# Kernel optimization log

Hardware: AMD Instinct MI355X
Metric: run time of the kernel (lower is better)

## Reference

```python
import jax, jax.numpy as jnp
import numpy as np

N = 50000      # points
K = 16         # neighbors per point
DIM = 256      # channels
H = 8          # heads
HD = DIM // H  # head dim


def setup_inputs() -> dict:
    key = jax.random.key(0)
    ks = jax.random.split(key, 8)
    feats = jax.random.normal(ks[0], (N, DIM), jnp.float32)
    xyz = jax.random.normal(ks[1], (N, 3), jnp.float32)
    # sorted segment ids: each point attends to exactly K neighbors
    index_0 = jnp.repeat(jnp.arange(N, dtype=jnp.int32), K)            # [M]
    index_1 = jax.random.randint(ks[2], (N * K,), 0, N, dtype=jnp.int32)  # [M]
    index_0_offsets = jnp.arange(N + 1, dtype=jnp.int32) * K
    s = 1.0 / np.sqrt(DIM)
    qkv_w = jax.random.normal(ks[3], (3 * DIM, DIM), jnp.float32) * s
    qkv_b = jax.random.normal(ks[4], (3 * DIM,), jnp.float32) * 0.01
    proj_w = jax.random.normal(ks[5], (DIM, DIM), jnp.float32) * s
    proj_b = jax.random.normal(ks[6], (DIM,), jnp.float32) * 0.01
    return {
        'feats': feats, 'xyz': xyz,
        'index_0': index_0, 'index_1': index_1,
        'index_0_offsets': index_0_offsets, 'n_max': K,
        'qkv_w': qkv_w, 'qkv_b': qkv_b, 'proj_w': proj_w, 'proj_b': proj_b,
    }


def reference(feats, xyz, index_0, index_1, index_0_offsets, n_max,
              qkv_w, qkv_b, proj_w, proj_b):
    n, c = feats.shape
    scale = (c // H) ** (-0.5)
    qkv = (feats @ qkv_w.T + qkv_b).reshape(n, 3, H, HD)  # [N,3,H,HD]
    q = qkv[:, 0] * scale
    k = qkv[:, 1]
    v = qkv[:, 2]
    # attention_step1: per-pair gathered dot product -> [M, H]
    attn = jnp.einsum('mhd,mhd->mh', q[index_0], k[index_1])
    # scatter_softmax over segments of index_0 (numerically stable)
    seg_max = jax.ops.segment_max(attn, index_0, num_segments=n)  # [N,H]
    e = jnp.exp(attn - seg_max[index_0])
    denom = jax.ops.segment_sum(e, index_0, num_segments=n)       # [N,H]
    attn = e / denom[index_0]                                     # [M,H]
    # attention_step2: scatter weighted sum of gathered values -> [N,H,HD]
    x = jax.ops.segment_sum(attn[:, :, None] * v[index_1], index_0,
                            num_segments=n)
    x = x.reshape(n, c)
    return x @ proj_w.T + proj_b
```

## Files before the change

### kernel.cpp

```cpp
#include <hip/hip_runtime.h>
#include <hip/hip_bf16.h>
#include <stdint.h>

typedef __bf16 bf16x8_t __attribute__((ext_vector_type(8)));
typedef float f32x4_t __attribute__((ext_vector_type(4)));

__device__ __forceinline__ float b2f(unsigned short u) {
    union { uint32_t i; float f; } x; x.i = ((uint32_t)u) << 16; return x.f;
}
__device__ __forceinline__ unsigned short f2b(float f) {
    union { float f; uint32_t i; } x; x.f = f;
    uint32_t r = (x.i + 0x7fffu + ((x.i >> 16) & 1u)) >> 16;
    return (unsigned short)r;
}

__global__ void cvt_f32_bf16(const float* __restrict__ in, unsigned short* __restrict__ out, int n) {
    int i = (blockIdx.x * blockDim.x + threadIdx.x) * 4;
    if (i >= n) return;
    const float4 v = *reinterpret_cast<const float4*>(in + i);
    ushort4 o;
    o.x = f2b(v.x); o.y = f2b(v.y); o.z = f2b(v.z); o.w = f2b(v.w);
    *reinterpret_cast<ushort4*>(out + i) = o;
}

template <bool OUT_BF16>
__launch_bounds__(256, 2)
__global__ void gemm_bf16(const unsigned short* __restrict__ A,
                          const unsigned short* __restrict__ W,
                          const float* __restrict__ bias,
                          void* __restrict__ Cout,
                          int M, int Nn, int Kk) {
    const int nCol = Nn >> 7;
    const int p = blockIdx.x;
    const int xcd = p & 7;
    const int q = p >> 3;
    const int c = q % nCol;
    const int rr = q / nCol;
    const int r = rr * 8 + xcd;
    const int blockRow = r * 128;
    if (blockRow >= M) return;
    const int blockCol = c * 128;

    __shared__ unsigned short As[128 * 64];
    __shared__ unsigned short Bs[128 * 64];
    const int t = threadIdx.x;
    const int w = t >> 6;
    const int l = t & 63;
    const int wm = w >> 1, wn = w & 1;

    f32x4_t acc[4][4];
#pragma unroll
    for (int i = 0; i < 4; ++i)
#pragma unroll
        for (int j = 0; j < 4; ++j) acc[i][j] = (f32x4_t)0.f;

    const int srow = t >> 3;
    const int scol = (t & 7) * 8;

    for (int k0 = 0; k0 < Kk; k0 += 64) {
#pragma unroll
        for (int cc = 0; cc < 4; ++cc) {
            int arow = blockRow + cc * 32 + srow;
            arow = arow < M ? arow : M - 1;
            const unsigned short* ga = A + (size_t)arow * Kk + k0 + scol;
            const int brow = blockCol + cc * 32 + srow;
            const unsigned short* gb = W + (size_t)brow * Kk + k0 + scol;
            unsigned short* la = &As[cc * 2048 + w * 512];
            unsigned short* lb = &Bs[cc * 2048 + w * 512];
            __builtin_amdgcn_global_load_lds((const __attribute__((address_space(1))) void*)ga,
                                             (__attribute__((address_space(3))) void*)la, 16, 0, 0);
            __builtin_amdgcn_global_load_lds((const __attribute__((address_space(1))) void*)gb,
                                             (__attribute__((address_space(3))) void*)lb, 16, 0, 0);
        }
        __syncthreads();
#pragma unroll
        for (int kc = 0; kc < 2; ++kc) {
            bf16x8_t af[4], bfr[4];
            const int kof = kc * 32 + (l >> 4) * 8;
#pragma unroll
            for (int i = 0; i < 4; ++i) {
                af[i]  = *reinterpret_cast<const bf16x8_t*>(&As[(wm * 64 + i * 16 + (l & 15)) * 64 + kof]);
                bfr[i] = *reinterpret_cast<const bf16x8_t*>(&Bs[(wn * 64 + i * 16 + (l & 15)) * 64 + kof]);
            }
#pragma unroll
            for (int i = 0; i < 4; ++i)
#pragma unroll
                for (int j = 0; j < 4; ++j)
                    acc[i][j] = __builtin_amdgcn_mfma_f32_16x16x32_bf16(af[i], bfr[j], acc[i][j], 0, 0, 0);
        }
        __syncthreads();
    }

    const int lr = (l >> 4) * 4;
    const int lc = l & 15;
#pragma unroll
    for (int i = 0; i < 4; ++i) {
#pragma unroll
        for (int j = 0; j < 4; ++j) {
            const int col = blockCol + wn * 64 + j * 16 + lc;
            const float bz = bias[col];
#pragma unroll
            for (int rg = 0; rg < 4; ++rg) {
                const int row = blockRow + wm * 64 + i * 16 + lr + rg;
                if (row < M) {
                    const float val = acc[i][j][rg] + bz;
                    if (OUT_BF16)
                        ((unsigned short*)Cout)[(size_t)row * Nn + col] = f2b(val);
                    else
                        ((float*)Cout)[(size_t)row * Nn + col] = val;
                }
            }
        }
    }
}

__global__ void attn_bf16(const unsigned short* __restrict__ qkv,
                          const int* __restrict__ index_1,
                          unsigned short* __restrict__ x) {
    const int w = threadIdx.x >> 6;
    const int i = blockIdx.x * 4 + w;
    const int l = threadIdx.x & 63;
    const int h = l >> 3;
    const int d0 = (l & 7) * 4;
    const float scale = 0.17677669529663687f;

    int nbr[16];
#pragma unroll
    for (int m = 0; m < 16; ++m) nbr[m] = index_1[i * 16 + m];

    ushort4 kreg[16], vreg[16];
#pragma unroll
    for (int m = 0; m < 16; ++m) {
        const unsigned short* base = qkv + (size_t)nbr[m] * 768 + 256 + h * 32 + d0;
        kreg[m] = *reinterpret_cast<const ushort4*>(base);
        vreg[m] = *reinterpret_cast<const ushort4*>(base + 256);
    }

    const ushort4 qu = *reinterpret_cast<const ushort4*>(&qkv[(size_t)i * 768 + h * 32 + d0]);
    const float qx = b2f(qu.x) * scale, qy = b2f(qu.y) * scale,
                qz = b2f(qu.z) * scale, qw = b2f(qu.w) * scale;

    float s[16];
#pragma unroll
    for (int m = 0; m < 16; ++m) {
        float p = qx * b2f(kreg[m].x) + qy * b2f(kreg[m].y)
                + qz * b2f(kreg[m].z) + qw * b2f(kreg[m].w);
        p += __shfl_xor(p, 1, 8);
        p += __shfl_xor(p, 2, 8);
        p += __shfl_xor(p, 4, 8);
        s[m] = p;
    }
    float mx = -1e30f;
#pragma unroll
    for (int m = 0; m < 16; ++m) mx = fmaxf(mx, s[m]);
    float sum = 0.f;
#pragma unroll
    for (int m = 0; m < 16; ++m) { s[m] = __expf(s[m] - mx); sum += s[m]; }
    const float inv = 1.f / sum;

    float ax = 0.f, ay = 0.f, az = 0.f, aw = 0.f;
#pragma unroll
    for (int m = 0; m < 16; ++m) {
        const float wt = s[m] * inv;
        ax += wt * b2f(vreg[m].x); ay += wt * b2f(vreg[m].y);
        az += wt * b2f(vreg[m].z); aw += wt * b2f(vreg[m].w);
    }
    ushort4 o;
    o.x = f2b(ax); o.y = f2b(ay); o.z = f2b(az); o.w = f2b(aw);
    *reinterpret_cast<ushort4*>(&x[(size_t)i * 256 + h * 32 + d0]) = o;
}

extern "C" void kernel_launch(void* const* d_in, const int* in_sizes, int n_in,
                              void* d_out, int out_size, void* d_ws, size_t ws_size,
                              hipStream_t stream) {
    const float* feats   = (const float*)d_in[0];
    const int*   index_1 = (const int*)d_in[3];
    const float* qkv_w   = (const float*)d_in[6];
    const float* qkv_b   = (const float*)d_in[7];
    const float* proj_w  = (const float*)d_in[8];
    const float* proj_b  = (const float*)d_in[9];
    float* out = (float*)d_out;

    const int N = 50000, DIM = 256, QKVD = 768;

    unsigned short* featsb = (unsigned short*)d_ws;
    unsigned short* qkvwb  = featsb + (size_t)N * DIM;
    unsigned short* projwb = qkvwb + (size_t)QKVD * DIM;
    unsigned short* qkvb   = projwb + (size_t)DIM * DIM;
    unsigned short* xb     = qkvb + (size_t)N * QKVD;

    cvt_f32_bf16<<<(N * DIM / 4 + 255) / 256, 256, 0, stream>>>(feats, featsb, N * DIM);
    cvt_f32_bf16<<<(QKVD * DIM / 4 + 255) / 256, 256, 0, stream>>>(qkv_w, qkvwb, QKVD * DIM);
    cvt_f32_bf16<<<(DIM * DIM / 4 + 255) / 256, 256, 0, stream>>>(proj_w, projwb, DIM * DIM);

    const int nRow = (N + 127) / 128;
    const int nRowPad = ((nRow + 7) / 8) * 8;

    gemm_bf16<true><<<nRowPad * (QKVD / 128), 256, 0, stream>>>(featsb, qkvwb, qkv_b, qkvb, N, QKVD, DIM);
    attn_bf16<<<N / 4, 256, 0, stream>>>(qkvb, index_1, xb);
    gemm_bf16<false><<<nRowPad * (DIM / 128), 256, 0, stream>>>(xb, projwb, proj_b, out, N, DIM, DIM);
}
```

Measured before the change: 309.7 us.

## Split QKV into separate planes and attention into logits and output kernels

The QKV GEMM now writes Q, K and V to three separate contiguous [N,256] bf16 arrays, so each gathered row comes from a smaller array. The attention kernel is split in two: one computes softmax weights from gathered K and stores them as packed bf16, the other gathers V and accumulates the weighted sum. The softmax scale is folded into the Q weights and bias inside a merged weight-prep kernel, and the weights are kept in bf16. This is meant to improve cache locality of the random gathers, at the cost of an extra launch, a second read of index_1, and an extra round trip for the weights.

```diff
diff --git a/kernel.cpp b/kernel.cpp
--- a/kernel.cpp
+++ b/kernel.cpp
@@ -13,6 +13,8 @@
     uint32_t r = (x.i + 0x7fffu + ((x.i >> 16) & 1u)) >> 16;
     return (unsigned short)r;
 }
+
+#define QSCALE 0.17677669529663687f
 
 __global__ void cvt_f32_bf16(const float* __restrict__ in, unsigned short* __restrict__ out, int n) {
     int i = (blockIdx.x * blockDim.x + threadIdx.x) * 4;
@@ -23,7 +25,33 @@
     *reinterpret_cast<ushort4*>(out + i) = o;
 }
 
-template <bool OUT_BF16>
+__global__ void prep_weights(const float* __restrict__ qkv_w, const float* __restrict__ proj_w,
+                             const float* __restrict__ qkv_b,
+                             unsigned short* __restrict__ qkvwb, unsigned short* __restrict__ projwb,
+                             float* __restrict__ qkvbS) {
+    const int idx = blockIdx.x * 256 + threadIdx.x;
+    if (idx < 49152) {
+        const int e = idx * 4;
+        const float4 v = *reinterpret_cast<const float4*>(qkv_w + e);
+        const float sc = (e >> 8) < 256 ? QSCALE : 1.f;
+        ushort4 o;
+        o.x = f2b(v.x * sc); o.y = f2b(v.y * sc); o.z = f2b(v.z * sc); o.w = f2b(v.w * sc);
+        *reinterpret_cast<ushort4*>(qkvwb + e) = o;
+    } else if (idx < 49152 + 16384) {
+        const int e = (idx - 49152) * 4;
+        const float4 v = *reinterpret_cast<const float4*>(proj_w + e);
+        ushort4 o;
+        o.x = f2b(v.x); o.y = f2b(v.y); o.z = f2b(v.z); o.w = f2b(v.w);
+        *reinterpret_cast<ushort4*>(projwb + e) = o;
+    } else if (idx < 49152 + 16384 + 192) {
+        const int e = (idx - 49152 - 16384) * 4;
+        float4 v = *reinterpret_cast<const float4*>(qkv_b + e);
+        if (e < 256) { v.x *= QSCALE; v.y *= QSCALE; v.z *= QSCALE; v.w *= QSCALE; }
+        *reinterpret_cast<float4*>(qkvbS + e) = v;
+    }
+}
+
+template <int OUT_MODE>
 __launch_bounds__(256, 2)
 __global__ void gemm_bf16(const unsigned short* __restrict__ A,
                           const unsigned short* __restrict__ W,
@@ -104,51 +132,50 @@
                 const int row = blockRow + wm * 64 + i * 16 + lr + rg;
                 if (row < M) {
                     const float val = acc[i][j][rg] + bz;
-                    if (OUT_BF16)
-                        ((unsigned short*)Cout)[(size_t)row * Nn + col] = f2b(val);
-                    else
+                    if (OUT_MODE == 0) {
                         ((float*)Cout)[(size_t)row * Nn + col] = val;
+                    } else {
+                        const size_t sec = (size_t)(col >> 8) * (size_t)M * 256;
+                        ((unsigned short*)Cout)[sec + (size_t)row * 256 + (col & 255)] = f2b(val);
+                    }
                 }
             }
         }
     }
 }
 
-__global__ void attn_bf16(const unsigned short* __restrict__ qkv,
-                          const int* __restrict__ index_1,
-                          unsigned short* __restrict__ x) {
+__global__ void attn_logits(const unsigned short* __restrict__ qb,
+                            const unsigned short* __restrict__ kb,
+                            const int* __restrict__ index_1,
+                            unsigned short* __restrict__ wbuf) {
     const int w = threadIdx.x >> 6;
     const int i = blockIdx.x * 4 + w;
     const int l = threadIdx.x & 63;
     const int h = l >> 3;
-    const int d0 = (l & 7) * 4;
-    const float scale = 0.17677669529663687f;
+    const int p = l & 7;
+    const int d0 = p * 4;
 
     int nbr[16];
 #pragma unroll
     for (int m = 0; m < 16; ++m) nbr[m] = index_1[i * 16 + m];
 
-    ushort4 kreg[16], vreg[16];
+    ushort4 kreg[16];
+#pragma unroll
+    for (int m = 0; m < 16; ++m)
+        kreg[m] = *reinterpret_cast<const ushort4*>(&kb[(size_t)nbr[m] * 256 + h * 32 + d0]);
+
+    const ushort4 qu = *reinterpret_cast<const ushort4*>(&qb[(size_t)i * 256 + h * 32 + d0]);
+    const float qx = b2f(qu.x), qy = b2f(qu.y), qz = b2f(qu.z), qw = b2f(qu.w);
+
+    float s[16];
 #pragma unroll
     for (int m = 0; m < 16; ++m) {
-        const unsigned short* base = qkv + (size_t)nbr[m] * 768 + 256 + h * 32 + d0;
-        kreg[m] = *reinterpret_cast<const ushort4*>(base);
-        vreg[m] = *reinterpret_cast<const ushort4*>(base + 256);
-    }
-
-    const ushort4 qu = *reinterpret_cast<const ushort4*>(&qkv[(size_t)i * 768 + h * 32 + d0]);
-    const float qx = b2f(qu.x) * scale, qy = b2f(qu.y) * scale,
-                qz = b2f(qu.z) * scale, qw = b2f(qu.w) * scale;
-
-    float s[16];
-#pragma unroll
-    for (int m = 0; m < 16; ++m) {
-        float p = qx * b2f(kreg[m].x) + qy * b2f(kreg[m].y)
-                + qz * b2f(kreg[m].z) + qw * b2f(kreg[m].w);
-        p += __shfl_xor(p, 1, 8);
-        p += __shfl_xor(p, 2, 8);
-        p += __shfl_xor(p, 4, 8);
-        s[m] = p;
+        float pv = qx * b2f(kreg[m].x) + qy * b2f(kreg[m].y)
+                 + qz * b2f(kreg[m].z) + qw * b2f(kreg[m].w);
+        pv += __shfl_xor(pv, 1, 8);
+        pv += __shfl_xor(pv, 2, 8);
+        pv += __shfl_xor(pv, 4, 8);
+        s[m] = pv;
     }
     float mx = -1e30f;
 #pragma unroll
@@ -158,16 +185,43 @@
     for (int m = 0; m < 16; ++m) { s[m] = __expf(s[m] - mx); sum += s[m]; }
     const float inv = 1.f / sum;
 
+    const uint32_t pack = (uint32_t)f2b(s[2 * p] * inv) | ((uint32_t)f2b(s[2 * p + 1] * inv) << 16);
+    ((uint32_t*)wbuf)[(size_t)i * 64 + h * 8 + p] = pack;
+}
+
+__global__ void attn_out(const unsigned short* __restrict__ vb,
+                         const unsigned short* __restrict__ wbuf,
+                         const int* __restrict__ index_1,
+                         unsigned short* __restrict__ xb) {
+    const int w = threadIdx.x >> 6;
+    const int i = blockIdx.x * 4 + w;
+    const int l = threadIdx.x & 63;
+    const int h = l >> 3;
+    const int p = l & 7;
+    const int d0 = p * 4;
+
+    int nbr[16];
+#pragma unroll
+    for (int m = 0; m < 16; ++m) nbr[m] = index_1[i * 16 + m];
+
+    ushort4 vreg[16];
+#pragma unroll
+    for (int m = 0; m < 16; ++m)
+        vreg[m] = *reinterpret_cast<const ushort4*>(&vb[(size_t)nbr[m] * 256 + h * 32 + d0]);
+
+    const uint32_t wp = ((const uint32_t*)wbuf)[(size_t)i * 64 + h * 8 + p];
+
     float ax = 0.f, ay = 0.f, az = 0.f, aw = 0.f;
 #pragma unroll
     for (int m = 0; m < 16; ++m) {
-        const float wt = s[m] * inv;
+        const uint32_t src = __shfl(wp, h * 8 + (m >> 1), 64);
+        const float wt = b2f((unsigned short)((m & 1) ? (src >> 16) : (src & 0xffff)));
         ax += wt * b2f(vreg[m].x); ay += wt * b2f(vreg[m].y);
         az += wt * b2f(vreg[m].z); aw += wt * b2f(vreg[m].w);
     }
     ushort4 o;
     o.x = f2b(ax); o.y = f2b(ay); o.z = f2b(az); o.w = f2b(aw);
-    *reinterpret_cast<ushort4*>(&x[(size_t)i * 256 + h * 32 + d0]) = o;
+    *reinterpret_cast<ushort4*>(&xb[(size_t)i * 256 + h * 32 + d0]) = o;
 }
 
 extern "C" void kernel_launch(void* const* d_in, const int* in_sizes, int n_in,
@@ -186,17 +240,22 @@
     unsigned short* featsb = (unsigned short*)d_ws;
     unsigned short* qkvwb  = featsb + (size_t)N * DIM;
     unsigned short* projwb = qkvwb + (size_t)QKVD * DIM;
-    unsigned short* qkvb   = projwb + (size_t)DIM * DIM;
-    unsigned short* xb     = qkvb + (size_t)N * QKVD;
+    float*          qkvbS  = (float*)(projwb + (size_t)DIM * DIM);
+    unsigned short* qb     = (unsigned short*)(qkvbS + QKVD);
+    unsigned short* kb     = qb + (size_t)N * DIM;
+    unsigned short* vb     = kb + (size_t)N * DIM;
+    unsigned short* xb     = vb + (size_t)N * DIM;
+    unsigned short* wbuf   = xb + (size_t)N * DIM;
 
     cvt_f32_bf16<<<(N * DIM / 4 + 255) / 256, 256, 0, stream>>>(feats, featsb, N * DIM);
-    cvt_f32_bf16<<<(QKVD * DIM / 4 + 255) / 256, 256, 0, stream>>>(qkv_w, qkvwb, QKVD * DIM);
-    cvt_f32_bf16<<<(DIM * DIM / 4 + 255) / 256, 256, 0, stream>>>(proj_w, projwb, DIM * DIM);
+    prep_weights<<<(49152 + 16384 + 192 + 255) / 256, 256, 0, stream>>>(
+        qkv_w, proj_w, qkv_b, qkvwb, projwb, qkvbS);
 
     const int nRow = (N + 127) / 128;
     const int nRowPad = ((nRow + 7) / 8) * 8;
 
-    gemm_bf16<true><<<nRowPad * (QKVD / 128), 256, 0, stream>>>(featsb, qkvwb, qkv_b, qkvb, N, QKVD, DIM);
-    attn_bf16<<<N / 4, 256, 0, stream>>>(qkvb, index_1, xb);
-    gemm_bf16<false><<<nRowPad * (DIM / 128), 256, 0, stream>>>(xb, projwb, proj_b, out, N, DIM, DIM);
-}
+    gemm_bf16<1><<<nRowPad * (QKVD / 128), 256, 0, stream>>>(featsb, qkvwb, qkvbS, qb, N, QKVD, DIM);
+    attn_logits<<<N / 4, 256, 0, stream>>>(qb, kb, index_1, wbuf);
+    attn_out<<<N / 4, 256, 0, stream>>>(vb, wbuf, index_1, xb);
+    gemm_bf16<0><<<nRowPad * (DIM / 128), 256, 0, stream>>>(xb, projwb, proj_b, out, N, DIM, DIM);
+}
```

Measured after the change: 307.4 us. About the same (-0.7%).
